# Performance work log

Measured on AMD Instinct MI355X. Metric: run time of the kernel, lower is better.

The kernel has to match this reference:

```python
import jax, jax.numpy as jnp
import numpy as np
import math

B, T, DP = 8, 512, 150
H = 512   # encoder hidden
HD = 512  # decoder hidden
L = 2     # layers per stack
NH = 8    # heads
R = 4     # downsample rate
E = 512   # embedding (code) dim
K = 4096  # codebook size
FF = 2048 # 4*hidden
COMMIT = 0.25

def _pe(seq_len, d):
    pos = np.arange(seq_len, dtype=np.float32)[:, None]
    div = np.exp(np.arange(0, d, 2, dtype=np.float32) * (-math.log(10000.0) / d))
    pe = np.zeros((seq_len, d), dtype=np.float32)
    pe[:, 0::2] = np.sin(pos * div)
    pe[:, 1::2] = np.cos(pos * div)
    return jnp.asarray(pe)

def _ln(x, w, b, eps=1e-5):
    m = x.mean(-1, keepdims=True)
    v = x.var(-1, keepdims=True)
    return (x - m) / jnp.sqrt(v + eps) * w + b

def _mha(q_in, kv_in, w_qkv, b_qkv, w_out, b_out, nh):
    d = q_in.shape[-1]
    wq, wk, wv = jnp.split(w_qkv, 3, axis=0)
    bq, bk, bv = jnp.split(b_qkv, 3, axis=0)
    q = q_in @ wq.T + bq
    k = kv_in @ wk.T + bk
    v = kv_in @ wv.T + bv
    b, sq, _ = q.shape
    sk = k.shape[1]
    dh = d // nh
    q = q.reshape(b, sq, nh, dh)
    k = k.reshape(b, sk, nh, dh)
    v = v.reshape(b, sk, nh, dh)
    att = jnp.einsum('bqhd,bkhd->bhqk', q, k) / jnp.sqrt(jnp.asarray(dh, q.dtype))
    p = jax.nn.softmax(att, axis=-1)
    o = jnp.einsum('bhqk,bkhd->bqhd', p, v).reshape(b, sq, d)
    return o @ w_out.T + b_out

def _ffn(x, w1, b1, w2, b2):
    return jax.nn.gelu(x @ w1.T + b1, approximate=False) @ w2.T + b2

def _forward(x, mask, enc_in_w, enc_in_b, enc_qkv_w, enc_qkv_b, enc_ao_w, enc_ao_b, enc_ln1_w, enc_ln1_b, enc_ln2_w, enc_ln2_b, enc_ff1_w, enc_ff1_b, enc_ff2_w, enc_ff2_b, enc_fln_w, enc_fln_b, enc_conv_w, enc_conv_b, codebook, dec_in_w, dec_in_b, dec_up_w, dec_up_b, query_emb, dec_sa_qkv_w, dec_sa_qkv_b, dec_sa_o_w, dec_sa_o_b, dec_ca_qkv_w, dec_ca_qkv_b, dec_ca_o_w, dec_ca_o_b, dec_ln1_w, dec_ln1_b, dec_ln2_w, dec_ln2_b, dec_ln3_w, dec_ln3_b, dec_ff1_w, dec_ff1_b, dec_ff2_w, dec_ff2_b, dec_out_w, dec_out_b):
    Bx, Tx, _ = x.shape
    # ----- MotionEncoder (pre-norm transformer encoder) -----
    h = x @ enc_in_w.T + enc_in_b + _pe(Tx, H)
    for i in range(L):
        y = _ln(h, enc_ln1_w[i], enc_ln1_b[i])
        h = h + _mha(y, y, enc_qkv_w[i], enc_qkv_b[i], enc_ao_w[i], enc_ao_b[i], NH)
        y = _ln(h, enc_ln2_w[i], enc_ln2_b[i])
        h = h + _ffn(y, enc_ff1_w[i], enc_ff1_b[i], enc_ff2_w[i], enc_ff2_b[i])
    h = _ln(h, enc_fln_w, enc_fln_b)
    # strided Conv1d (kernel=stride=R) temporal downsample; weight (E, H, R)
    hr = h.reshape(Bx, Tx // R, R, H)
    z_e = jnp.einsum('btrh,ehr->bte', hr, enc_conv_w) + enc_conv_b  # (B, T//R, E)
    # ----- VectorQuantizer (eval path: cdist + argmin + gather) -----
    flat = z_e.reshape(-1, E)
    dist = (flat * flat).sum(1, keepdims=True) + (codebook * codebook).sum(1) - 2.0 * (flat @ codebook.T)
    idx = jnp.argmin(dist, axis=1)
    quantized = codebook[idx].reshape(z_e.shape)
    e_latent = jnp.mean((jax.lax.stop_gradient(quantized) - z_e) ** 2)
    vq_loss = COMMIT * e_latent
    z_q = z_e + jax.lax.stop_gradient(quantized - z_e)  # straight-through
    # ----- MotionDecoder -----
    mem = z_q @ dec_in_w.T + dec_in_b
    # ConvTranspose1d (kernel=stride=R) temporal upsample; weight (HD_in, HD_out, R)
    mem = (jnp.einsum('btc,cok->btko', mem, dec_up_w) + dec_up_b).reshape(Bx, -1, HD)
    tgt_len = Tx  # mask is all-ones so target_length == T (static)
    mem = mem[:, :tgt_len] + _pe(tgt_len, HD)
    q = query_emb[None, :tgt_len] + _pe(tgt_len, HD)
    q = jnp.broadcast_to(q, (Bx, tgt_len, HD))
    for i in range(L):
        y = _ln(q, dec_ln1_w[i], dec_ln1_b[i])
        q = q + _mha(y, y, dec_sa_qkv_w[i], dec_sa_qkv_b[i], dec_sa_o_w[i], dec_sa_o_b[i], NH)
        y = _ln(q, dec_ln2_w[i], dec_ln2_b[i])
        q = q + _mha(y, mem, dec_ca_qkv_w[i], dec_ca_qkv_b[i], dec_ca_o_w[i], dec_ca_o_b[i], NH)
        y = _ln(q, dec_ln3_w[i], dec_ln3_b[i])
        q = q + _ffn(y, dec_ff1_w[i], dec_ff1_b[i], dec_ff2_w[i], dec_ff2_b[i])
    recon = q @ dec_out_w.T + dec_out_b
    valid = mask[..., None].astype(recon.dtype)
    recon_loss = jnp.sum((recon * valid - x * valid) ** 2) / jnp.maximum(valid.sum(), 1.0)
    return recon, idx.reshape(Bx, Tx // R), recon_loss, vq_loss, e_latent, z_e

def setup_inputs() -> dict:
    key = jax.random.key(0)
    ks = iter(jax.random.split(key, 64))
    def rn(shape, s=0.05):
        return jax.random.normal(next(ks), shape, dtype=jnp.float32) * s
    return {
        'x': jax.random.normal(next(ks), (B, T, DP), dtype=jnp.float32),
        'mask': jnp.ones((B, T), dtype=bool),
        'enc_in_w': rn((H, DP)), 'enc_in_b': jnp.zeros((H,), jnp.float32),
        'enc_qkv_w': rn((L, 3 * H, H)), 'enc_qkv_b': jnp.zeros((L, 3 * H), jnp.float32),
        'enc_ao_w': rn((L, H, H)), 'enc_ao_b': jnp.zeros((L, H), jnp.float32),
        'enc_ln1_w': jnp.ones((L, H), jnp.float32), 'enc_ln1_b': jnp.zeros((L, H), jnp.float32),
        'enc_ln2_w': jnp.ones((L, H), jnp.float32), 'enc_ln2_b': jnp.zeros((L, H), jnp.float32),
        'enc_ff1_w': rn((L, FF, H)), 'enc_ff1_b': jnp.zeros((L, FF), jnp.float32),
        'enc_ff2_w': rn((L, H, FF)), 'enc_ff2_b': jnp.zeros((L, H), jnp.float32),
        'enc_fln_w': jnp.ones((H,), jnp.float32), 'enc_fln_b': jnp.zeros((H,), jnp.float32),
        'enc_conv_w': rn((E, H, R)), 'enc_conv_b': jnp.zeros((E,), jnp.float32),
        'codebook': jax.random.uniform(next(ks), (K, E), dtype=jnp.float32, minval=-1.0 / K, maxval=1.0 / K),
        'dec_in_w': rn((HD, E)), 'dec_in_b': jnp.zeros((HD,), jnp.float32),
        'dec_up_w': rn((HD, HD, R)), 'dec_up_b': jnp.zeros((HD,), jnp.float32),
        'query_emb': rn((T, HD), 1.0),
        'dec_sa_qkv_w': rn((L, 3 * HD, HD)), 'dec_sa_qkv_b': jnp.zeros((L, 3 * HD), jnp.float32),
        'dec_sa_o_w': rn((L, HD, HD)), 'dec_sa_o_b': jnp.zeros((L, HD), jnp.float32),
        'dec_ca_qkv_w': rn((L, 3 * HD, HD)), 'dec_ca_qkv_b': jnp.zeros((L, 3 * HD), jnp.float32),
        'dec_ca_o_w': rn((L, HD, HD)), 'dec_ca_o_b': jnp.zeros((L, HD), jnp.float32),
        'dec_ln1_w': jnp.ones((L, HD), jnp.float32), 'dec_ln1_b': jnp.zeros((L, HD), jnp.float32),
        'dec_ln2_w': jnp.ones((L, HD), jnp.float32), 'dec_ln2_b': jnp.zeros((L, HD), jnp.float32),
        'dec_ln3_w': jnp.ones((L, HD), jnp.float32), 'dec_ln3_b': jnp.zeros((L, HD), jnp.float32),
        'dec_ff1_w': rn((L, FF, HD)), 'dec_ff1_b': jnp.zeros((L, FF), jnp.float32),
        'dec_ff2_w': rn((L, HD, FF)), 'dec_ff2_b': jnp.zeros((L, HD), jnp.float32),
        'dec_out_w': rn((DP, HD)), 'dec_out_b': jnp.zeros((DP,), jnp.float32),
    }

def reference(x, mask, enc_in_w, enc_in_b, enc_qkv_w, enc_qkv_b, enc_ao_w, enc_ao_b, enc_ln1_w, enc_ln1_b, enc_ln2_w, enc_ln2_b, enc_ff1_w, enc_ff1_b, enc_ff2_w, enc_ff2_b, enc_fln_w, enc_fln_b, enc_conv_w, enc_conv_b, codebook, dec_in_w, dec_in_b, dec_up_w, dec_up_b, query_emb, dec_sa_qkv_w, dec_sa_qkv_b, dec_sa_o_w, dec_sa_o_b, dec_ca_qkv_w, dec_ca_qkv_b, dec_ca_o_w, dec_ca_o_b, dec_ln1_w, dec_ln1_b, dec_ln2_w, dec_ln2_b, dec_ln3_w, dec_ln3_b, dec_ff1_w, dec_ff1_b, dec_ff2_w, dec_ff2_b, dec_out_w, dec_out_b):
    return _forward(x, mask, enc_in_w, enc_in_b, enc_qkv_w, enc_qkv_b, enc_ao_w, enc_ao_b, enc_ln1_w, enc_ln1_b, enc_ln2_w, enc_ln2_b, enc_ff1_w, enc_ff1_b, enc_ff2_w, enc_ff2_b, enc_fln_w, enc_fln_b, enc_conv_w, enc_conv_b, codebook, dec_in_w, dec_in_b, dec_up_w, dec_up_b, query_emb, dec_sa_qkv_w, dec_sa_qkv_b, dec_sa_o_w, dec_sa_o_b, dec_ca_qkv_w, dec_ca_qkv_b, dec_ca_o_w, dec_ca_o_b, dec_ln1_w, dec_ln1_b, dec_ln2_w, dec_ln2_b, dec_ln3_w, dec_ln3_b, dec_ff1_w, dec_ff1_b, dec_ff2_w, dec_ff2_b, dec_out_w, dec_out_b)
```

## Files before the change

### kernel.cpp

```cpp
#include <hip/hip_runtime.h>
#include <hip/hip_bf16.h>
#include <math.h>

namespace {
constexpr int kT    = 512;
constexpr int kH    = 512;
constexpr int kFF   = 2048;
constexpr int kB    = 8;
constexpr int kNTOK = kB * kT;
constexpr int kNLAT = kB * kT / 4;
constexpr int kK    = 4096;
constexpr int kDP   = 150;
constexpr long kReconN  = (long)kNTOK * kDP;
constexpr long kIdxOff  = kReconN;
constexpr long kScalOff = kReconN + kNLAT;
constexpr long kZeOff   = kScalOff + 3;
constexpr long kZeN     = (long)kNLAT * 512;
}

typedef __attribute__((ext_vector_type(8))) short bf16x8;
typedef __attribute__((ext_vector_type(4))) float f32x4;
typedef unsigned short u16;

__device__ inline u16 f2bf(float f) {
  __hip_bfloat16 h = __float2bfloat16(f);
  return *reinterpret_cast<u16*>(&h);
}


__global__ __launch_bounds__(256) void zero_scal_kernel(float* s) {
  if (threadIdx.x < 2) s[threadIdx.x] = 0.0f;
}

__global__ __launch_bounds__(256) void pe_kernel(float* __restrict__ pe) {
  int i = blockIdx.x * 256 + threadIdx.x;
  int t = i >> 9, c = i & 511;
  int j2 = c & ~1;
  double div = exp((double)j2 * (-9.210340371976184 / 512.0));
  double a = (double)t * div;
  pe[i] = (float)((c & 1) ? cos(a) : sin(a));
}

__global__ __launch_bounds__(256) void addpe_kernel(float* __restrict__ h, const float* __restrict__ pe) {
  long i = (long)blockIdx.x * 256 + threadIdx.x;
  h[i] += pe[i & (long)(kT * kH - 1)];
}

__global__ __launch_bounds__(256) void qinit_kernel(float* __restrict__ q, const float* __restrict__ qe,
                                                    const float* __restrict__ pe) {
  long i = (long)blockIdx.x * 256 + threadIdx.x;
  long j = i & (long)(kT * kH - 1);
  q[i] = qe[j] + pe[j];
}

__global__ __launch_bounds__(256) void perm_encconv_kernel(const float* __restrict__ w, float* __restrict__ W2) {
  int i = blockIdx.x * 256 + threadIdx.x;
  int e = i >> 11, rem = i & 2047, r = rem >> 9, hh = rem & 511;
  W2[i] = w[e * 2048 + hh * 4 + r];
}

__global__ __launch_bounds__(256) void perm_decup_kernel(const float* __restrict__ w, const float* __restrict__ bvec,
                                                         float* __restrict__ W3, float* __restrict__ B3) {
  int i = blockIdx.x * 256 + threadIdx.x;
  int n = i >> 9, c = i & 511, kk = n >> 9, o = n & 511;
  W3[i] = w[c * 2048 + o * 4 + kk];
  if (c == 0) B3[n] = bvec[o];
}


__global__ __launch_bounds__(256) void ln_kernel(const float* __restrict__ X, const float* __restrict__ w,
                                                 const float* __restrict__ b, float* __restrict__ Y) {
  __shared__ double red[256];
  long row = blockIdx.x;
  const float* x = X + row * 512;
  float* y = Y + row * 512;
  int tid = threadIdx.x;
  float v0 = x[tid], v1 = x[tid + 256];
  red[tid] = (double)v0 + (double)v1; __syncthreads();
  for (int s = 128; s > 0; s >>= 1) { if (tid < s) red[tid] += red[tid + s]; __syncthreads(); }
  double mean = red[0] * (1.0 / 512.0);
  __syncthreads();
  double d0 = (double)v0 - mean, d1 = (double)v1 - mean;
  red[tid] = d0 * d0 + d1 * d1; __syncthreads();
  for (int s = 128; s > 0; s >>= 1) { if (tid < s) red[tid] += red[tid + s]; __syncthreads(); }
  double var = red[0] * (1.0 / 512.0);
  double inv = 1.0 / sqrt(var + 1e-5);
  y[tid]       = (float)(d0 * inv * (double)w[tid]       + (double)b[tid]);
  y[tid + 256] = (float)(d1 * inv * (double)w[tid + 256] + (double)b[tid + 256]);
}


__global__ __launch_bounds__(256) void softmax_rows_kernel(float* __restrict__ S) {
  __shared__ double red[256];
  long row = blockIdx.x;
  float* p = S + row * 512;
  int tid = threadIdx.x;
  float v0 = p[tid], v1 = p[tid + 256];
  red[tid] = (double)fmaxf(v0, v1); __syncthreads();
  for (int s = 128; s > 0; s >>= 1) { if (tid < s) red[tid] = fmax(red[tid], red[tid + s]); __syncthreads(); }
  float m = (float)red[0];
  __syncthreads();
  float e0 = expf(v0 - m), e1 = expf(v1 - m);
  red[tid] = (double)e0 + (double)e1; __syncthreads();
  for (int s = 128; s > 0; s >>= 1) { if (tid < s) red[tid] += red[tid + s]; __syncthreads(); }
  double inv = 1.0 / red[0];
  p[tid] = (float)(e0 * inv); p[tid + 256] = (float)(e1 * inv);
}


__global__ __launch_bounds__(256) void gemm64_k(
    const float* __restrict__ A, int lda, long sAo, long sAi,
    const float* __restrict__ W, int ldw, long sWo, long sWi,
    float* __restrict__ C, int ldc, long sCo, long sCi,
    const float* __restrict__ bias,
    int M, int N, int Kd, int zDiv, float alpha, int flags) {
  int z = blockIdx.z;
  int zo = z / zDiv, zi = z % zDiv;
  A += (long)zo * sAo + (long)zi * sAi;
  W += (long)zo * sWo + (long)zi * sWi;
  C += (long)zo * sCo + (long)zi * sCi;
  __shared__ float As[32][64];
  __shared__ float Ws[32][64];
  int tid = threadIdx.x;
  int tx = tid & 15, ty = tid >> 4;
  int rowBase = blockIdx.y * 64, colBase = blockIdx.x * 64;
  bool vec4 = ((lda & 3) == 0) && ((ldw & 3) == 0) && ((Kd & 3) == 0);
  double acc[4][4] = {};
  for (int kb = 0; kb < Kd; kb += 32) {
    int r = tid >> 2, s = (tid & 3) << 3;
    int ga = rowBase + r;
    int gw = colBase + r;
    if (vec4 && (kb + 32 <= Kd)) {
      float4 va0 = make_float4(0.f, 0.f, 0.f, 0.f), va1 = va0, vw0 = va0, vw1 = va0;
      if (ga < M) {
        va0 = *reinterpret_cast<const float4*>(A + (long)ga * lda + kb + s);
        va1 = *reinterpret_cast<const float4*>(A + (long)ga * lda + kb + s + 4);
      }
      if (gw < N) {
        vw0 = *reinterpret_cast<const float4*>(W + (long)gw * ldw + kb + s);
        vw1 = *reinterpret_cast<const float4*>(W + (long)gw * ldw + kb + s + 4);
      }
      As[s + 0][r] = va0.x; As[s + 1][r] = va0.y; As[s + 2][r] = va0.z; As[s + 3][r] = va0.w;
      As[s + 4][r] = va1.x; As[s + 5][r] = va1.y; As[s + 6][r] = va1.z; As[s + 7][r] = va1.w;
      Ws[s + 0][r] = vw0.x; Ws[s + 1][r] = vw0.y; Ws[s + 2][r] = vw0.z; Ws[s + 3][r] = vw0.w;
      Ws[s + 4][r] = vw1.x; Ws[s + 5][r] = vw1.y; Ws[s + 6][r] = vw1.z; Ws[s + 7][r] = vw1.w;
    } else {
#pragma unroll
      for (int q2 = 0; q2 < 8; ++q2) {
        int k = kb + s + q2;
        As[s + q2][r] = (ga < M && k < Kd) ? A[(long)ga * lda + k] : 0.f;
        Ws[s + q2][r] = (gw < N && k < Kd) ? W[(long)gw * ldw + k] : 0.f;
      }
    }
    __syncthreads();
#pragma unroll
    for (int kk = 0; kk < 32; ++kk) {
      double a[4], w[4];
#pragma unroll
      for (int u = 0; u < 4; ++u) { a[u] = (double)As[kk][(ty << 2) + u]; w[u] = (double)Ws[kk][(tx << 2) + u]; }
#pragma unroll
      for (int i2 = 0; i2 < 4; ++i2)
#pragma unroll
        for (int j2 = 0; j2 < 4; ++j2)
          acc[i2][j2] += a[i2] * w[j2];
    }
    __syncthreads();
  }
#pragma unroll
  for (int i2 = 0; i2 < 4; ++i2) {
    int r = rowBase + (ty << 2) + i2;
    if (r >= M) continue;
#pragma unroll
    for (int j2 = 0; j2 < 4; ++j2) {
      int cidx = colBase + (tx << 2) + j2;
      if (cidx >= N) continue;
      double v = (double)alpha * acc[i2][j2];
      if (bias) v += (double)bias[cidx];
      if (flags & 2) v = 0.5 * v * (1.0 + erf(v * 0.7071067811865475244));
      long o = (long)r * ldc + cidx;
      if (flags & 1) v += (double)C[o];
      C[o] = (float)v;
    }
  }
}


__global__ __launch_bounds__(256) void pv64_k(const float* __restrict__ P, const float* __restrict__ V, int ldv,
                                              float* __restrict__ O) {
  int z = blockIdx.z;
  int bz = z >> 3, h = z & 7;
  const float* Pz = P + (long)z * (kT * kT);
  const float* Vz = V + (long)bz * kT * ldv + h * 64;
  float* Oz = O + (long)bz * kT * 512 + h * 64;
  int ib = blockIdx.x * 64;
  __shared__ float Ps[16][64];
  __shared__ float Vs[16][64];
  int tid = threadIdx.x;
  int tx = tid & 15, ty = tid >> 4;
  double acc[4][4] = {};
  for (int jb = 0; jb < kT; jb += 16) {
    {
      int i = tid >> 2;
      int seg = (tid & 3) << 2;
      float4 v = *reinterpret_cast<const float4*>(Pz + (long)(ib + i) * kT + jb + seg);
      Ps[seg + 0][i] = v.x; Ps[seg + 1][i] = v.y; Ps[seg + 2][i] = v.z; Ps[seg + 3][i] = v.w;
      int j = tid >> 4;
      int dseg = (tid & 15) << 2;
      float4 w = *reinterpret_cast<const float4*>(Vz + (long)(jb + j) * ldv + dseg);
      *reinterpret_cast<float4*>(&Vs[j][dseg]) = w;
    }
    __syncthreads();
#pragma unroll
    for (int kk = 0; kk < 16; ++kk) {
      double a[4], w[4];
#pragma unroll
      for (int u = 0; u < 4; ++u) { a[u] = (double)Ps[kk][(ty << 2) + u]; w[u] = (double)Vs[kk][(tx << 2) + u]; }
#pragma unroll
      for (int i2 = 0; i2 < 4; ++i2)
#pragma unroll
        for (int j2 = 0; j2 < 4; ++j2)
          acc[i2][j2] += a[i2] * w[j2];
    }
    __syncthreads();
  }
#pragma unroll
  for (int i2 = 0; i2 < 4; ++i2)
#pragma unroll
    for (int j2 = 0; j2 < 4; ++j2)
      Oz[(long)(ib + (ty << 2) + i2) * 512 + (tx << 2) + j2] = (float)acc[i2][j2];
}


__global__ __launch_bounds__(256) void mgemm_k(
    const float* __restrict__ A, int lda,
    const float* __restrict__ W, int ldw,
    float* __restrict__ C, int ldc,
    const float* __restrict__ bias,
    int M, int N, int Kd, float alpha, int flags) {
  __shared__ __align__(16) u16 As[64][40];
  __shared__ __align__(16) u16 Ws[64][40];
  int tid = threadIdx.x;
  int rowBase = blockIdx.y * 64, colBase = blockIdx.x * 64;
  int wv = tid >> 6, lane = tid & 63;
  int wr = (wv >> 1) << 5, wc = (wv & 1) << 5;
  int fr = lane & 15, fs = lane >> 4;
  f32x4 acc[2][2] = {};
  for (int kb = 0; kb < Kd; kb += 32) {
    int r = tid >> 2, kq = (tid & 3) << 3;
    {
      int ga = rowBase + r;
      float4 v0 = make_float4(0.f, 0.f, 0.f, 0.f), v1 = v0;
      if (ga < M) {
        v0 = *reinterpret_cast<const float4*>(A + (long)ga * lda + kb + kq);
        v1 = *reinterpret_cast<const float4*>(A + (long)ga * lda + kb + kq + 4);
      }
      u16* d = &As[r][kq];
      d[0] = f2bf(v0.x); d[1] = f2bf(v0.y); d[2] = f2bf(v0.z); d[3] = f2bf(v0.w);
      d[4] = f2bf(v1.x); d[5] = f2bf(v1.y); d[6] = f2bf(v1.z); d[7] = f2bf(v1.w);
    }
    {
      int gw = colBase + r;
      float4 v0 = make_float4(0.f, 0.f, 0.f, 0.f), v1 = v0;
      if (gw < N) {
        v0 = *reinterpret_cast<const float4*>(W + (long)gw * ldw + kb + kq);
        v1 = *reinterpret_cast<const float4*>(W + (long)gw * ldw + kb + kq + 4);
      }
      u16* d = &Ws[r][kq];
      d[0] = f2bf(v0.x); d[1] = f2bf(v0.y); d[2] = f2bf(v0.z); d[3] = f2bf(v0.w);
      d[4] = f2bf(v1.x); d[5] = f2bf(v1.y); d[6] = f2bf(v1.z); d[7] = f2bf(v1.w);
    }
    __syncthreads();
    bf16x8 af0 = *reinterpret_cast<const bf16x8*>(&As[wr + fr][fs << 3]);
    bf16x8 af1 = *reinterpret_cast<const bf16x8*>(&As[wr + 16 + fr][fs << 3]);
    bf16x8 bf0 = *reinterpret_cast<const bf16x8*>(&Ws[wc + fr][fs << 3]);
    bf16x8 bf1 = *reinterpret_cast<const bf16x8*>(&Ws[wc + 16 + fr][fs << 3]);
    acc[0][0] = __builtin_amdgcn_mfma_f32_16x16x32_bf16(af0, bf0, acc[0][0], 0, 0, 0);
    acc[0][1] = __builtin_amdgcn_mfma_f32_16x16x32_bf16(af0, bf1, acc[0][1], 0, 0, 0);
    acc[1][0] = __builtin_amdgcn_mfma_f32_16x16x32_bf16(af1, bf0, acc[1][0], 0, 0, 0);
    acc[1][1] = __builtin_amdgcn_mfma_f32_16x16x32_bf16(af1, bf1, acc[1][1], 0, 0, 0);
    __syncthreads();
  }
#pragma unroll
  for (int i = 0; i < 2; ++i) {
#pragma unroll
    for (int j = 0; j < 2; ++j) {
#pragma unroll
      for (int r = 0; r < 4; ++r) {
        int row = rowBase + wr + i * 16 + fs * 4 + r;
        int col = colBase + wc + j * 16 + fr;
        if (row < M && col < N) {
          float v = alpha * acc[i][j][r];
          if (bias) v += bias[col];
          if (flags & 2) v = 0.5f * v * (1.0f + erff(v * 0.7071067811865475f));
          long o = (long)row * ldc + col;
          if (flags & 1) v += C[o];
          C[o] = v;
        }
      }
    }
  }
}


__global__ __launch_bounds__(256) void flash_attn_k(const float* __restrict__ QKV, float* __restrict__ O) {
  int qc = blockIdx.x, h = blockIdx.y, b = blockIdx.z;
  const float* Qg = QKV + ((long)b * 512 + qc * 128) * 1536 + h * 64;
  const float* Kg = QKV + ((long)b * 512) * 1536 + 512 + h * 64;
  const float* Vg = QKV + ((long)b * 512) * 1536 + 1024 + h * 64;
  float* Og = O + ((long)b * 512 + qc * 128) * 512 + h * 64;
  __shared__ __align__(16) u16 Qs[128][72];
  __shared__ __align__(16) u16 Ks[64][72];
  __shared__ __align__(16) u16 Vt[64][72];
  __shared__ __align__(16) u16 Pstg[4][32][72];
  int tid = threadIdx.x;
  int wv = tid >> 6, lane = tid & 63;
  int fr = lane & 15, fs = lane >> 4;
  int q0 = wv * 32;
  {
    int r = tid >> 1, c0 = (tid & 1) * 32;
#pragma unroll
    for (int e = 0; e < 8; ++e) {
      float4 v = *reinterpret_cast<const float4*>(Qg + (long)r * 1536 + c0 + e * 4);
      u16* d = &Qs[r][c0 + e * 4];
      d[0] = f2bf(v.x * 0.125f); d[1] = f2bf(v.y * 0.125f);
      d[2] = f2bf(v.z * 0.125f); d[3] = f2bf(v.w * 0.125f);
    }
  }
  float m[2][4], l[2][4];
  f32x4 o_[2][4] = {};
#pragma unroll
  for (int a = 0; a < 2; ++a)
#pragma unroll
    for (int r = 0; r < 4; ++r) { m[a][r] = -1e30f; l[a][r] = 0.0f; }
  __syncthreads();
  for (int kt = 0; kt < 8; ++kt) {
    int j0 = kt * 64;
    {
      int r = tid >> 2, c0 = (tid & 3) * 16;
#pragma unroll
      for (int e = 0; e < 4; ++e) {
        float4 v = *reinterpret_cast<const float4*>(Kg + (long)(j0 + r) * 1536 + c0 + e * 4);
        u16* d = &Ks[r][c0 + e * 4];
        d[0] = f2bf(v.x); d[1] = f2bf(v.y); d[2] = f2bf(v.z); d[3] = f2bf(v.w);
      }
      int j = tid >> 2, d0 = (tid & 3) * 16;
#pragma unroll
      for (int e = 0; e < 4; ++e) {
        float4 v = *reinterpret_cast<const float4*>(Vg + (long)(j0 + j) * 1536 + d0 + e * 4);
        Vt[d0 + e * 4 + 0][j] = f2bf(v.x);
        Vt[d0 + e * 4 + 1][j] = f2bf(v.y);
        Vt[d0 + e * 4 + 2][j] = f2bf(v.z);
        Vt[d0 + e * 4 + 3][j] = f2bf(v.w);
      }
    }
    __syncthreads();
    f32x4 s[2][4] = {};
#pragma unroll
    for (int rf = 0; rf < 2; ++rf) {
      bf16x8 a0 = *reinterpret_cast<const bf16x8*>(&Qs[q0 + rf * 16 + fr][fs << 3]);
      bf16x8 a1 = *reinterpret_cast<const bf16x8*>(&Qs[q0 + rf * 16 + fr][32 + (fs << 3)]);
#pragma unroll
      for (int cf = 0; cf < 4; ++cf) {
        bf16x8 b0 = *reinterpret_cast<const bf16x8*>(&Ks[cf * 16 + fr][fs << 3]);
        bf16x8 b1 = *reinterpret_cast<const bf16x8*>(&Ks[cf * 16 + fr][32 + (fs << 3)]);
        s[rf][cf] = __builtin_amdgcn_mfma_f32_16x16x32_bf16(a0, b0, s[rf][cf], 0, 0, 0);
        s[rf][cf] = __builtin_amdgcn_mfma_f32_16x16x32_bf16(a1, b1, s[rf][cf], 0, 0, 0);
      }
    }
#pragma unroll
    for (int rf = 0; rf < 2; ++rf) {
#pragma unroll
      for (int r = 0; r < 4; ++r) {
        float mt = fmaxf(fmaxf(s[rf][0][r], s[rf][1][r]), fmaxf(s[rf][2][r], s[rf][3][r]));
        mt = fmaxf(mt, __shfl_xor(mt, 1, 64));
        mt = fmaxf(mt, __shfl_xor(mt, 2, 64));
        mt = fmaxf(mt, __shfl_xor(mt, 4, 64));
        mt = fmaxf(mt, __shfl_xor(mt, 8, 64));
        float mn = fmaxf(m[rf][r], mt);
        float sc = expf(m[rf][r] - mn);
        m[rf][r] = mn;
        float rs = 0.0f;
        int prow = rf * 16 + fs * 4 + r;
#pragma unroll
        for (int cf = 0; cf < 4; ++cf) {
          float p = expf(s[rf][cf][r] - mn);
          rs += p;
          Pstg[wv][prow][cf * 16 + fr] = f2bf(p);
        }
        rs += __shfl_xor(rs, 1, 64);
        rs += __shfl_xor(rs, 2, 64);
        rs += __shfl_xor(rs, 4, 64);
        rs += __shfl_xor(rs, 8, 64);
        l[rf][r] = l[rf][r] * sc + rs;
#pragma unroll
        for (int df = 0; df < 4; ++df) o_[rf][df][r] *= sc;
      }
    }
    __syncthreads();
#pragma unroll
    for (int rf = 0; rf < 2; ++rf) {
      bf16x8 pa0 = *reinterpret_cast<const bf16x8*>(&Pstg[wv][rf * 16 + fr][fs << 3]);
      bf16x8 pa1 = *reinterpret_cast<const bf16x8*>(&Pstg[wv][rf * 16 + fr][32 + (fs << 3)]);
#pragma unroll
      for (int df = 0; df < 4; ++df) {
        bf16x8 vb0 = *reinterpret_cast<const bf16x8*>(&Vt[df * 16 + fr][fs << 3]);
        bf16x8 vb1 = *reinterpret_cast<const bf16x8*>(&Vt[df * 16 + fr][32 + (fs << 3)]);
        o_[rf][df] = __builtin_amdgcn_mfma_f32_16x16x32_bf16(pa0, vb0, o_[rf][df], 0, 0, 0);
        o_[rf][df] = __builtin_amdgcn_mfma_f32_16x16x32_bf16(pa1, vb1, o_[rf][df], 0, 0, 0);
      }
    }
    __syncthreads();
  }
#pragma unroll
  for (int rf = 0; rf < 2; ++rf) {
#pragma unroll
    for (int r = 0; r < 4; ++r) {
      float inv = 1.0f / l[rf][r];
      int row = q0 + rf * 16 + fs * 4 + r;
#pragma unroll
      for (int df = 0; df < 4; ++df)
        Og[(long)row * 512 + df * 16 + fr] = o_[rf][df][r] * inv;
    }
  }
}


__global__ __launch_bounds__(256) void codenorm_f_kernel(const float* __restrict__ cb, float* __restrict__ cnf) {
  __shared__ double red[256];
  int j = blockIdx.x;
  const float* c = cb + (long)j * 512;
  int tid = threadIdx.x;
  float s0 = c[tid] * c[tid];
  float s1 = c[tid + 256] * c[tid + 256];
  red[tid] = (double)s0 + (double)s1; __syncthreads();
  for (int s = 128; s > 0; s >>= 1) { if (tid < s) red[tid] += red[tid + s]; __syncthreads(); }
  if (tid == 0) cnf[j] = (float)red[0];
}

__global__ __launch_bounds__(256) void vq_argmin_kernel(const float* __restrict__ ze, const float* __restrict__ D,
                                                        const float* __restrict__ cnf,
                                                        int* __restrict__ idx_out, float* __restrict__ idx_f) {
  __shared__ double redd[256];
  __shared__ float bv[256];
  __shared__ int bis[256];
  __shared__ float AfS;
  int row = blockIdx.x;
  int tid = threadIdx.x;
  const float* zr = ze + (long)row * 512;
  float z0 = zr[tid], z1 = zr[tid + 256];
  redd[tid] = (double)(z0 * z0) + (double)(z1 * z1);
  __syncthreads();
  for (int s = 128; s > 0; s >>= 1) { if (tid < s) redd[tid] += redd[tid + s]; __syncthreads(); }
  if (tid == 0) AfS = (float)redd[0];
  __syncthreads();
  float Af = AfS;
  const float* dr = D + (long)row * kK;
  float best = INFINITY; int bi = 0;
  for (int j = tid; j < kK; j += 256) {
    float dd = (Af + cnf[j]) - dr[j];
    if (dd < best) { best = dd; bi = j; }
  }
  bv[tid] = best; bis[tid] = bi; __syncthreads();
  for (int s = 128; s > 0; s >>= 1) {
    if (tid < s) {
      if (bv[tid + s] < bv[tid] || (bv[tid + s] == bv[tid] && bis[tid + s] < bis[tid])) {
        bv[tid] = bv[tid + s]; bis[tid] = bis[tid + s];
      }
    }
    __syncthreads();
  }
  if (tid == 0) { idx_out[row] = bis[0]; idx_f[row] = (float)bis[0]; }
}

__global__ __launch_bounds__(256) void gather_kernel(const float* __restrict__ cb, const int* __restrict__ idx,
                                                     const float* __restrict__ ze, float* __restrict__ zq,
                                                     float* __restrict__ ze_out, float* __restrict__ scal) {
  __shared__ float red[256];
  long i = (long)blockIdx.x * 256 + threadIdx.x;
  int row = (int)(i >> 9), c = (int)(i & 511);
  float q = cb[(long)idx[row] * 512 + c];
  float zv = ze[i];
  zq[i] = q;
  ze_out[i] = zv;
  float dsq = (q - zv) * (q - zv);
  red[threadIdx.x] = dsq; __syncthreads();
  for (int s = 128; s > 0; s >>= 1) { if (threadIdx.x < s) red[threadIdx.x] += red[threadIdx.x + s]; __syncthreads(); }
  if (threadIdx.x == 0) atomicAdd(&scal[1], red[0]);
}


__global__ __launch_bounds__(256) void recon_out_kernel(const float* __restrict__ recon, const float* __restrict__ x,
                                                        float* __restrict__ out, float* __restrict__ scal) {
  __shared__ float red[256];
  long i = (long)blockIdx.x * 256 + threadIdx.x;
  float r = recon[i];
  out[i] = r;
  float d = r - x[i];
  red[threadIdx.x] = d * d; __syncthreads();
  for (int s = 128; s > 0; s >>= 1) { if (threadIdx.x < s) red[threadIdx.x] += red[threadIdx.x + s]; __syncthreads(); }
  if (threadIdx.x == 0) atomicAdd(&scal[0], red[0]);
}

__global__ void finalize_kernel(const float* __restrict__ scal, float* __restrict__ out) {
  float rl = scal[0] / 4096.0f;
  float el = scal[1] / (float)kZeN;
  out[kScalOff + 0] = rl;
  out[kScalOff + 1] = 0.25f * el;
  out[kScalOff + 2] = el;
}


extern "C" void kernel_launch(void* const* d_in, const int* in_sizes, int n_in,
                              void* d_out, int out_size, void* d_ws, size_t ws_size,
                              hipStream_t stream) {
  (void)out_size; (void)ws_size;
  int base = 2;
  for (int i = 1; i <= 3 && i + 1 < n_in; ++i) {
    if (in_sizes[i] == 76800 && in_sizes[i + 1] == 512) { base = i; break; }
  }
  const int off = base - 2;

  const float* x          = (const float*)d_in[0];
  const float* enc_in_w   = (const float*)d_in[2 + off];
  const float* enc_in_b   = (const float*)d_in[3 + off];
  const float* enc_qkv_w  = (const float*)d_in[4 + off];
  const float* enc_qkv_b  = (const float*)d_in[5 + off];
  const float* enc_ao_w   = (const float*)d_in[6 + off];
  const float* enc_ao_b   = (const float*)d_in[7 + off];
  const float* enc_ln1_w  = (const float*)d_in[8 + off];
  const float* enc_ln1_b  = (const float*)d_in[9 + off];
  const float* enc_ln2_w  = (const float*)d_in[10 + off];
  const float* enc_ln2_b  = (const float*)d_in[11 + off];
  const float* enc_ff1_w  = (const float*)d_in[12 + off];
  const float* enc_ff1_b  = (const float*)d_in[13 + off];
  const float* enc_ff2_w  = (const float*)d_in[14 + off];
  const float* enc_ff2_b  = (const float*)d_in[15 + off];
  const float* enc_fln_w  = (const float*)d_in[16 + off];
  const float* enc_fln_b  = (const float*)d_in[17 + off];
  const float* enc_conv_w = (const float*)d_in[18 + off];
  const float* enc_conv_b = (const float*)d_in[19 + off];
  const float* codebook   = (const float*)d_in[20 + off];
  const float* dec_in_w   = (const float*)d_in[21 + off];
  const float* dec_in_b   = (const float*)d_in[22 + off];
  const float* dec_up_w   = (const float*)d_in[23 + off];
  const float* dec_up_b   = (const float*)d_in[24 + off];
  const float* query_emb  = (const float*)d_in[25 + off];
  const float* dec_sa_qkv_w = (const float*)d_in[26 + off];
  const float* dec_sa_qkv_b = (const float*)d_in[27 + off];
  const float* dec_sa_o_w   = (const float*)d_in[28 + off];
  const float* dec_sa_o_b   = (const float*)d_in[29 + off];
  const float* dec_ca_qkv_w = (const float*)d_in[30 + off];
  const float* dec_ca_qkv_b = (const float*)d_in[31 + off];
  const float* dec_ca_o_w   = (const float*)d_in[32 + off];
  const float* dec_ca_o_b   = (const float*)d_in[33 + off];
  const float* dec_ln1_w  = (const float*)d_in[34 + off];
  const float* dec_ln1_b  = (const float*)d_in[35 + off];
  const float* dec_ln2_w  = (const float*)d_in[36 + off];
  const float* dec_ln2_b  = (const float*)d_in[37 + off];
  const float* dec_ln3_w  = (const float*)d_in[38 + off];
  const float* dec_ln3_b  = (const float*)d_in[39 + off];
  const float* dec_ff1_w  = (const float*)d_in[40 + off];
  const float* dec_ff1_b  = (const float*)d_in[41 + off];
  const float* dec_ff2_w  = (const float*)d_in[42 + off];
  const float* dec_ff2_b  = (const float*)d_in[43 + off];
  const float* dec_out_w  = (const float*)d_in[44 + off];
  const float* dec_out_b  = (const float*)d_in[45 + off];

  float* outp = (float*)d_out;

  float* wsf   = (float*)d_ws;
  float* SCALp = wsf;
  float* CNFp  = wsf + 8;
  int*   IDXp  = (int*)(wsf + 8 + 4096);
  float* B3p   = wsf + 8 + 4096 + 1024;
  float* PEp   = wsf + 8192;
  float* Hp    = wsf + 270336;
  float* Yp    = wsf + 2367488;
  float* MEMp  = wsf + 4464640;
  float* ZEp   = wsf + 6561792;
  float* ZQp   = wsf + 7086080;
  float* BIGp  = wsf + 7610368;
  float* QKVp  = wsf + 9707520;
  float* SCp   = MEMp;

  auto gemm64 = [&](const float* A, int lda, const float* W, int ldw, float* C, int ldc,
                    const float* bias, int M, int N, int Kd, float alpha, int flags,
                    int nz = 1, int zDiv = 1,
                    long sAo = 0, long sAi = 0, long sWo = 0, long sWi = 0, long sCo = 0, long sCi = 0) {
    dim3 g((N + 63) / 64, (M + 63) / 64, nz);
    gemm64_k<<<g, 256, 0, stream>>>(A, lda, sAo, sAi, W, ldw, sWo, sWi, C, ldc, sCo, sCi,
                                    bias, M, N, Kd, zDiv, alpha, flags);
  };

  auto mgemm = [&](const float* A, int lda, const float* W, int ldw, float* C, int ldc,
                   const float* bias, int M, int N, int Kd, float alpha, int flags) {
    dim3 g((N + 63) / 64, (M + 63) / 64, 1);
    mgemm_k<<<g, 256, 0, stream>>>(A, lda, W, ldw, C, ldc, bias, M, N, Kd, alpha, flags);
  };

  auto ln = [&](const float* X, const float* w, const float* b, float* Y, int rows) {
    ln_kernel<<<rows, 256, 0, stream>>>(X, w, b, Y);
  };

  auto enc_attention = [&](const float* QKVbase, float* Ob) {
    for (int c2 = 0; c2 < 4; ++c2) {
      int b0 = c2 * 2;
      const float* QKVb = QKVbase + (long)b0 * kT * 1536;
      gemm64(QKVb, 1536, QKVb + 512, 1536, SCp, 512, nullptr,
             512, 512, 64, 0.125f, 0,
             16, 8, (long)kT * 1536, 64, (long)kT * 1536, 64,
             (long)8 * kT * kT, (long)kT * kT);
      softmax_rows_kernel<<<16 * kT, 256, 0, stream>>>(SCp);
      pv64_k<<<dim3(8, 1, 16), 256, 0, stream>>>(SCp, QKVb + 1024, 1536, Ob + (long)b0 * kT * 512);
    }
  };

  zero_scal_kernel<<<1, 256, 0, stream>>>(SCALp);
  pe_kernel<<<1024, 256, 0, stream>>>(PEp);

  gemm64(x, kDP, enc_in_w, kDP, Hp, 512, enc_in_b, kNTOK, 512, kDP, 1.f, 0);
  addpe_kernel<<<8192, 256, 0, stream>>>(Hp, PEp);

  for (int i = 0; i < 2; ++i) {
    ln(Hp, enc_ln1_w + i * 512, enc_ln1_b + i * 512, Yp, kNTOK);
    gemm64(Yp, 512, enc_qkv_w + (long)i * 1536 * 512, 512, QKVp, 1536,
           enc_qkv_b + i * 1536, kNTOK, 1536, 512, 1.f, 0);
    enc_attention(QKVp, Yp);
    gemm64(Yp, 512, enc_ao_w + (long)i * 262144, 512, Hp, 512, enc_ao_b + i * 512, kNTOK, 512, 512, 1.f, 1);
    ln(Hp, enc_ln2_w + i * 512, enc_ln2_b + i * 512, Yp, kNTOK);
    gemm64(Yp, 512, enc_ff1_w + (long)i * kFF * 512, 512, BIGp, kFF,
           enc_ff1_b + i * kFF, kNTOK, kFF, 512, 1.f, 2);
    gemm64(BIGp, kFF, enc_ff2_w + (long)i * 512 * kFF, kFF, Hp, 512,
           enc_ff2_b + i * 512, kNTOK, 512, kFF, 1.f, 1);
  }

  ln(Hp, enc_fln_w, enc_fln_b, Yp, kNTOK);
  perm_encconv_kernel<<<4096, 256, 0, stream>>>(enc_conv_w, BIGp);
  gemm64(Yp, 2048, BIGp, 2048, ZEp, 512, enc_conv_b, kNLAT, 512, 2048, 1.f, 0);

  codenorm_f_kernel<<<kK, 256, 0, stream>>>(codebook, CNFp);
  gemm64(ZEp, 512, codebook, 512, BIGp, kK, nullptr, kNLAT, kK, 512, 2.0f, 0);
  vq_argmin_kernel<<<kNLAT, 256, 0, stream>>>(ZEp, BIGp, CNFp, IDXp, outp + kIdxOff);
  gather_kernel<<<2048, 256, 0, stream>>>(codebook, IDXp, ZEp, ZQp, outp + kZeOff, SCALp);

  mgemm(ZQp, 512, dec_in_w, 512, Yp, 512, dec_in_b, kNLAT, 512, 512, 1.f, 0);
  perm_decup_kernel<<<4096, 256, 0, stream>>>(dec_up_w, dec_up_b, BIGp, B3p);
  mgemm(Yp, 512, BIGp, 512, MEMp, 2048, B3p, kNLAT, 2048, 512, 1.f, 0);
  addpe_kernel<<<8192, 256, 0, stream>>>(MEMp, PEp);
  qinit_kernel<<<8192, 256, 0, stream>>>(Hp, query_emb, PEp);

  for (int i = 0; i < 2; ++i) {
    ln(Hp, dec_ln1_w + i * 512, dec_ln1_b + i * 512, Yp, kNTOK);
    mgemm(Yp, 512, dec_sa_qkv_w + (long)i * 786432, 512, QKVp, 1536,
          dec_sa_qkv_b + i * 1536, kNTOK, 1536, 512, 1.f, 0);
    flash_attn_k<<<dim3(4, 8, 8), 256, 0, stream>>>(QKVp, Yp);
    mgemm(Yp, 512, dec_sa_o_w + (long)i * 262144, 512, Hp, 512,
          dec_sa_o_b + i * 512, kNTOK, 512, 512, 1.f, 1);
    ln(Hp, dec_ln2_w + i * 512, dec_ln2_b + i * 512, Yp, kNTOK);
    const float* caw = dec_ca_qkv_w + (long)i * 786432;
    const float* cab = dec_ca_qkv_b + i * 1536;
    mgemm(Yp,   512, caw,          512, QKVp,       1536, cab,       kNTOK, 512,  512, 1.f, 0);
    mgemm(MEMp, 512, caw + 262144, 512, QKVp + 512, 1536, cab + 512, kNTOK, 1024, 512, 1.f, 0);
    flash_attn_k<<<dim3(4, 8, 8), 256, 0, stream>>>(QKVp, Yp);
    mgemm(Yp, 512, dec_ca_o_w + (long)i * 262144, 512, Hp, 512,
          dec_ca_o_b + i * 512, kNTOK, 512, 512, 1.f, 1);
    ln(Hp, dec_ln3_w + i * 512, dec_ln3_b + i * 512, Yp, kNTOK);
    mgemm(Yp, 512, dec_ff1_w + (long)i * kFF * 512, 512, BIGp, kFF,
          dec_ff1_b + i * kFF, kNTOK, kFF, 512, 1.f, 2);
    mgemm(BIGp, kFF, dec_ff2_w + (long)i * 512 * kFF, kFF, Hp, 512,
          dec_ff2_b + i * 512, kNTOK, 512, kFF, 1.f, 1);
  }

  mgemm(Hp, 512, dec_out_w, 512, BIGp, kDP, dec_out_b, kNTOK, kDP, 512, 1.f, 0);
  recon_out_kernel<<<2400, 256, 0, stream>>>(BIGp, x, outp, SCALp);
  finalize_kernel<<<1, 1, 0, stream>>>(SCALp, outp);
}
```

Before: 3.300 ms.

## Use FP64 MFMA for double-accumulating GEMMs with runtime layout probe

Replaces the scalar double-precision FMA inner loop of the generic GEMM with v_mfma_f64_16x16x4f64 matrix instructions, each wave computing a 32x32 sub-tile. A one-wave probe kernel at startup tests 16 candidate operand and accumulator lane layouts against a scalar reference and writes the matching one to a workspace flag. The GEMM reads that flag and falls back to the old scalar path if no layout matched. This aims to cut the cost of the FP64 GEMMs while keeping double accumulation, at the price of an extra launch, a global flag read per block and a larger kernel with two code paths.

```diff
diff --git a/kernel.cpp b/kernel.cpp
--- a/kernel.cpp
+++ b/kernel.cpp
@@ -20,6 +20,7 @@
 
 typedef __attribute__((ext_vector_type(8))) short bf16x8;
 typedef __attribute__((ext_vector_type(4))) float f32x4;
+typedef __attribute__((ext_vector_type(4))) double f64x4;
 typedef unsigned short u16;
 
 __device__ inline u16 f2bf(float f) {
@@ -27,9 +28,62 @@
   return *reinterpret_cast<u16*>(&h);
 }
 
+__device__ inline void dmap_f64(int vd, int lane, int r, int* dm, int* dn) {
+  switch (vd) {
+    case 0: *dm = (lane >> 4) * 4 + r; *dn = lane & 15; break;
+    case 1: *dm = lane & 15;           *dn = (lane >> 4) * 4 + r; break;
+    case 2: *dm = (lane >> 4) + 4 * r; *dn = lane & 15; break;
+    default:*dm = lane & 15;           *dn = (lane >> 4) + 4 * r; break;
+  }
+}
+
 
 __global__ __launch_bounds__(256) void zero_scal_kernel(float* s) {
   if (threadIdx.x < 2) s[threadIdx.x] = 0.0f;
+}
+
+__global__ __launch_bounds__(64) void probe_f64_kernel(int* __restrict__ flag) {
+  __shared__ double Am[16][4], Bm[4][16], Am2[16][4], Bm2[4][16];
+  __shared__ double Cm[16][16], Ref[16][16];
+  int l = threadIdx.x;
+  {
+    int m = l & 15, k = l >> 4;
+    Am[m][k]  = 1.0 / (3.0 + (double)m + 17.0 * (double)k);
+    Am2[m][k] = 1.0 / (5.0 + 2.0 * (double)m + 13.0 * (double)k);
+    Bm[k][m]  = 1.0 / (7.0 + (double)m + 11.0 * (double)k);
+    Bm2[k][m] = 1.0 / (2.0 + 3.0 * (double)m + 19.0 * (double)k);
+  }
+  for (int e = l * 4; e < l * 4 + 4; ++e)
+    Cm[e >> 4][e & 15] = 1.0 / (1.0 + (double)(e >> 4) + 29.0 * (double)(e & 15));
+  __syncthreads();
+  for (int e = l * 4; e < l * 4 + 4; ++e) {
+    int mm = e >> 4, nn = e & 15;
+    double s = Cm[mm][nn];
+    for (int k = 0; k < 4; ++k) s = fma(Am[mm][k], Bm[k][nn], s);
+    for (int k = 0; k < 4; ++k) s = fma(Am2[mm][k], Bm2[k][nn], s);
+    Ref[mm][nn] = s;
+  }
+  __syncthreads();
+  int found = -1;
+  for (int v = 0; v < 16; ++v) {
+    int va = (v >> 3) & 1, vb = (v >> 2) & 1, vd = v & 3;
+    double a1 = va ? Am[l >> 2][l & 3]  : Am[l & 15][l >> 4];
+    double a2 = va ? Am2[l >> 2][l & 3] : Am2[l & 15][l >> 4];
+    double b1 = vb ? Bm[l & 3][l >> 2]  : Bm[l >> 4][l & 15];
+    double b2 = vb ? Bm2[l & 3][l >> 2] : Bm2[l >> 4][l & 15];
+    f64x4 d;
+    for (int r = 0; r < 4; ++r) { int dm, dn; dmap_f64(vd, l, r, &dm, &dn); d[r] = Cm[dm][dn]; }
+    d = __builtin_amdgcn_mfma_f64_16x16x4f64(a1, b1, d, 0, 0, 0);
+    d = __builtin_amdgcn_mfma_f64_16x16x4f64(a2, b2, d, 0, 0, 0);
+    bool ok = true;
+    for (int r = 0; r < 4; ++r) {
+      int dm, dn; dmap_f64(vd, l, r, &dm, &dn);
+      ok = ok && (d[r] == Ref[dm][dn]);
+    }
+    unsigned long long ball = __ballot(ok);
+    if (ball == 0xFFFFFFFFFFFFFFFFull && found < 0) found = v;
+  }
+  if (l == 0) *flag = found;
 }
 
 __global__ __launch_bounds__(256) void pe_kernel(float* __restrict__ pe) {
@@ -108,12 +162,13 @@
 }
 
 
-__global__ __launch_bounds__(256) void gemm64_k(
+__global__ __launch_bounds__(256) void dgemm_k(
     const float* __restrict__ A, int lda, long sAo, long sAi,
     const float* __restrict__ W, int ldw, long sWo, long sWi,
     float* __restrict__ C, int ldc, long sCo, long sCi,
     const float* __restrict__ bias,
-    int M, int N, int Kd, int zDiv, float alpha, int flags) {
+    int M, int N, int Kd, int zDiv, float alpha, int flags,
+    const int* __restrict__ flagp) {
   int z = blockIdx.z;
   int zo = z / zDiv, zi = z % zDiv;
   A += (long)zo * sAo + (long)zi * sAi;
@@ -122,64 +177,137 @@
   __shared__ float As[32][64];
   __shared__ float Ws[32][64];
   int tid = threadIdx.x;
-  int tx = tid & 15, ty = tid >> 4;
   int rowBase = blockIdx.y * 64, colBase = blockIdx.x * 64;
   bool vec4 = ((lda & 3) == 0) && ((ldw & 3) == 0) && ((Kd & 3) == 0);
-  double acc[4][4] = {};
-  for (int kb = 0; kb < Kd; kb += 32) {
-    int r = tid >> 2, s = (tid & 3) << 3;
-    int ga = rowBase + r;
-    int gw = colBase + r;
-    if (vec4 && (kb + 32 <= Kd)) {
-      float4 va0 = make_float4(0.f, 0.f, 0.f, 0.f), va1 = va0, vw0 = va0, vw1 = va0;
-      if (ga < M) {
-        va0 = *reinterpret_cast<const float4*>(A + (long)ga * lda + kb + s);
-        va1 = *reinterpret_cast<const float4*>(A + (long)ga * lda + kb + s + 4);
-      }
-      if (gw < N) {
-        vw0 = *reinterpret_cast<const float4*>(W + (long)gw * ldw + kb + s);
-        vw1 = *reinterpret_cast<const float4*>(W + (long)gw * ldw + kb + s + 4);
-      }
-      As[s + 0][r] = va0.x; As[s + 1][r] = va0.y; As[s + 2][r] = va0.z; As[s + 3][r] = va0.w;
-      As[s + 4][r] = va1.x; As[s + 5][r] = va1.y; As[s + 6][r] = va1.z; As[s + 7][r] = va1.w;
-      Ws[s + 0][r] = vw0.x; Ws[s + 1][r] = vw0.y; Ws[s + 2][r] = vw0.z; Ws[s + 3][r] = vw0.w;
-      Ws[s + 4][r] = vw1.x; Ws[s + 5][r] = vw1.y; Ws[s + 6][r] = vw1.z; Ws[s + 7][r] = vw1.w;
-    } else {
-#pragma unroll
-      for (int q2 = 0; q2 < 8; ++q2) {
-        int k = kb + s + q2;
-        As[s + q2][r] = (ga < M && k < Kd) ? A[(long)ga * lda + k] : 0.f;
-        Ws[s + q2][r] = (gw < N && k < Kd) ? W[(long)gw * ldw + k] : 0.f;
-      }
-    }
-    __syncthreads();
-#pragma unroll
-    for (int kk = 0; kk < 32; ++kk) {
-      double a[4], w[4];
-#pragma unroll
-      for (int u = 0; u < 4; ++u) { a[u] = (double)As[kk][(ty << 2) + u]; w[u] = (double)Ws[kk][(tx << 2) + u]; }
-#pragma unroll
-      for (int i2 = 0; i2 < 4; ++i2)
-#pragma unroll
-        for (int j2 = 0; j2 < 4; ++j2)
-          acc[i2][j2] += a[i2] * w[j2];
-    }
-    __syncthreads();
-  }
-#pragma unroll
-  for (int i2 = 0; i2 < 4; ++i2) {
-    int r = rowBase + (ty << 2) + i2;
-    if (r >= M) continue;
-#pragma unroll
-    for (int j2 = 0; j2 < 4; ++j2) {
-      int cidx = colBase + (tx << 2) + j2;
-      if (cidx >= N) continue;
-      double v = (double)alpha * acc[i2][j2];
-      if (bias) v += (double)bias[cidx];
-      if (flags & 2) v = 0.5 * v * (1.0 + erf(v * 0.7071067811865475244));
-      long o = (long)r * ldc + cidx;
-      if (flags & 1) v += (double)C[o];
-      C[o] = (float)v;
+  int mode = *flagp;
+
+  if (mode >= 0) {
+    int wv = tid >> 6, lane = tid & 63;
+    int wr = (wv >> 1) << 5, wc = (wv & 1) << 5;
+    int va = (mode >> 3) & 1, vb = (mode >> 2) & 1, vd = mode & 3;
+    int aM = va ? (lane >> 2) : (lane & 15);
+    int aK = va ? (lane & 3)  : (lane >> 4);
+    int bN = vb ? (lane >> 2) : (lane & 15);
+    int bK = vb ? (lane & 3)  : (lane >> 4);
+    int dmr[4], dnr[4];
+#pragma unroll
+    for (int r = 0; r < 4; ++r) dmap_f64(vd, lane, r, &dmr[r], &dnr[r]);
+    f64x4 acc[2][2] = {};
+    for (int kb = 0; kb < Kd; kb += 32) {
+      int r = tid >> 2, s = (tid & 3) << 3;
+      int ga = rowBase + r, gw = colBase + r;
+      if (vec4 && (kb + 32 <= Kd)) {
+        float4 va0 = make_float4(0.f, 0.f, 0.f, 0.f), va1 = va0, vw0 = va0, vw1 = va0;
+        if (ga < M) {
+          va0 = *reinterpret_cast<const float4*>(A + (long)ga * lda + kb + s);
+          va1 = *reinterpret_cast<const float4*>(A + (long)ga * lda + kb + s + 4);
+        }
+        if (gw < N) {
+          vw0 = *reinterpret_cast<const float4*>(W + (long)gw * ldw + kb + s);
+          vw1 = *reinterpret_cast<const float4*>(W + (long)gw * ldw + kb + s + 4);
+        }
+        As[s + 0][r] = va0.x; As[s + 1][r] = va0.y; As[s + 2][r] = va0.z; As[s + 3][r] = va0.w;
+        As[s + 4][r] = va1.x; As[s + 5][r] = va1.y; As[s + 6][r] = va1.z; As[s + 7][r] = va1.w;
+        Ws[s + 0][r] = vw0.x; Ws[s + 1][r] = vw0.y; Ws[s + 2][r] = vw0.z; Ws[s + 3][r] = vw0.w;
+        Ws[s + 4][r] = vw1.x; Ws[s + 5][r] = vw1.y; Ws[s + 6][r] = vw1.z; Ws[s + 7][r] = vw1.w;
+      } else {
+#pragma unroll
+        for (int q2 = 0; q2 < 8; ++q2) {
+          int k = kb + s + q2;
+          As[s + q2][r] = (ga < M && k < Kd) ? A[(long)ga * lda + k] : 0.f;
+          Ws[s + q2][r] = (gw < N && k < Kd) ? W[(long)gw * ldw + k] : 0.f;
+        }
+      }
+      __syncthreads();
+#pragma unroll
+      for (int c = 0; c < 8; ++c) {
+        double a0 = (double)As[c * 4 + aK][wr + aM];
+        double a1 = (double)As[c * 4 + aK][wr + 16 + aM];
+        double b0 = (double)Ws[c * 4 + bK][wc + bN];
+        double b1 = (double)Ws[c * 4 + bK][wc + 16 + bN];
+        acc[0][0] = __builtin_amdgcn_mfma_f64_16x16x4f64(a0, b0, acc[0][0], 0, 0, 0);
+        acc[0][1] = __builtin_amdgcn_mfma_f64_16x16x4f64(a0, b1, acc[0][1], 0, 0, 0);
+        acc[1][0] = __builtin_amdgcn_mfma_f64_16x16x4f64(a1, b0, acc[1][0], 0, 0, 0);
+        acc[1][1] = __builtin_amdgcn_mfma_f64_16x16x4f64(a1, b1, acc[1][1], 0, 0, 0);
+      }
+      __syncthreads();
+    }
+#pragma unroll
+    for (int i = 0; i < 2; ++i) {
+#pragma unroll
+      for (int j = 0; j < 2; ++j) {
+#pragma unroll
+        for (int r = 0; r < 4; ++r) {
+          int row = rowBase + wr + i * 16 + dmr[r];
+          int col = colBase + wc + j * 16 + dnr[r];
+          if (row < M && col < N) {
+            double v = (double)alpha * acc[i][j][r];
+            if (bias) v += (double)bias[col];
+            if (flags & 2) v = 0.5 * v * (1.0 + erf(v * 0.7071067811865475244));
+            long o = (long)row * ldc + col;
+            if (flags & 1) v += (double)C[o];
+            C[o] = (float)v;
+          }
+        }
+      }
+    }
+  } else {
+    int tx = tid & 15, ty = tid >> 4;
+    double acc[4][4] = {};
+    for (int kb = 0; kb < Kd; kb += 32) {
+      int r = tid >> 2, s = (tid & 3) << 3;
+      int ga = rowBase + r, gw = colBase + r;
+      if (vec4 && (kb + 32 <= Kd)) {
+        float4 va0 = make_float4(0.f, 0.f, 0.f, 0.f), va1 = va0, vw0 = va0, vw1 = va0;
+        if (ga < M) {
+          va0 = *reinterpret_cast<const float4*>(A + (long)ga * lda + kb + s);
+          va1 = *reinterpret_cast<const float4*>(A + (long)ga * lda + kb + s + 4);
+        }
+        if (gw < N) {
+          vw0 = *reinterpret_cast<const float4*>(W + (long)gw * ldw + kb + s);
+          vw1 = *reinterpret_cast<const float4*>(W + (long)gw * ldw + kb + s + 4);
+        }
+        As[s + 0][r] = va0.x; As[s + 1][r] = va0.y; As[s + 2][r] = va0.z; As[s + 3][r] = va0.w;
+        As[s + 4][r] = va1.x; As[s + 5][r] = va1.y; As[s + 6][r] = va1.z; As[s + 7][r] = va1.w;
+        Ws[s + 0][r] = vw0.x; Ws[s + 1][r] = vw0.y; Ws[s + 2][r] = vw0.z; Ws[s + 3][r] = vw0.w;
+        Ws[s + 4][r] = vw1.x; Ws[s + 5][r] = vw1.y; Ws[s + 6][r] = vw1.z; Ws[s + 7][r] = vw1.w;
+      } else {
+#pragma unroll
+        for (int q2 = 0; q2 < 8; ++q2) {
+          int k = kb + s + q2;
+          As[s + q2][r] = (ga < M && k < Kd) ? A[(long)ga * lda + k] : 0.f;
+          Ws[s + q2][r] = (gw < N && k < Kd) ? W[(long)gw * ldw + k] : 0.f;
+        }
+      }
+      __syncthreads();
+#pragma unroll
+      for (int kk = 0; kk < 32; ++kk) {
+        double a[4], w[4];
+#pragma unroll
+        for (int u = 0; u < 4; ++u) { a[u] = (double)As[kk][(ty << 2) + u]; w[u] = (double)Ws[kk][(tx << 2) + u]; }
+#pragma unroll
+        for (int i2 = 0; i2 < 4; ++i2)
+#pragma unroll
+          for (int j2 = 0; j2 < 4; ++j2)
+            acc[i2][j2] += a[i2] * w[j2];
+      }
+      __syncthreads();
+    }
+#pragma unroll
+    for (int i2 = 0; i2 < 4; ++i2) {
+      int r = rowBase + (ty << 2) + i2;
+      if (r >= M) continue;
+#pragma unroll
+      for (int j2 = 0; j2 < 4; ++j2) {
+        int cidx = colBase + (tx << 2) + j2;
+        if (cidx >= N) continue;
+        double v = (double)alpha * acc[i2][j2];
+        if (bias) v += (double)bias[cidx];
+        if (flags & 2) v = 0.5 * v * (1.0 + erf(v * 0.7071067811865475244));
+        long o = (long)r * ldc + cidx;
+        if (flags & 1) v += (double)C[o];
+        C[o] = (float)v;
+      }
     }
   }
 }
@@ -570,6 +698,7 @@
 
   float* wsf   = (float*)d_ws;
   float* SCALp = wsf;
+  int*   FLAGp = (int*)(wsf + 2);
   float* CNFp  = wsf + 8;
   int*   IDXp  = (int*)(wsf + 8 + 4096);
   float* B3p   = wsf + 8 + 4096 + 1024;
@@ -588,8 +717,8 @@
                     int nz = 1, int zDiv = 1,
                     long sAo = 0, long sAi = 0, long sWo = 0, long sWi = 0, long sCo = 0, long sCi = 0) {
     dim3 g((N + 63) / 64, (M + 63) / 64, nz);
-    gemm64_k<<<g, 256, 0, stream>>>(A, lda, sAo, sAi, W, ldw, sWo, sWi, C, ldc, sCo, sCi,
-                                    bias, M, N, Kd, zDiv, alpha, flags);
+    dgemm_k<<<g, 256, 0, stream>>>(A, lda, sAo, sAi, W, ldw, sWo, sWi, C, ldc, sCo, sCi,
+                                   bias, M, N, Kd, zDiv, alpha, flags, FLAGp);
   };
 
   auto mgemm = [&](const float* A, int lda, const float* W, int ldw, float* C, int ldc,
@@ -616,6 +745,7 @@
   };
 
   zero_scal_kernel<<<1, 256, 0, stream>>>(SCALp);
+  probe_f64_kernel<<<1, 64, 0, stream>>>(FLAGp);
   pe_kernel<<<1024, 256, 0, stream>>>(PEp);
 
   gemm64(x, kDP, enc_in_w, kDP, Hp, 512, enc_in_b, kNTOK, 512, kDP, 1.f, 0);
```

Result: faster. 3.115 ms (-5.6%).
